# Performance work log

Hardware: AMD Instinct MI355X
Metric: run time of the kernel (lower is better)

Reference implementation:

```python
import jax, jax.numpy as jnp
import numpy as np

B, H, W, C, HEADS, SR = 4, 64, 64, 256, 8, 2
D = C // HEADS            # head dim = 32
SCALE = D ** -0.5
EPS = 1e-6


def _conv(x, w, stride, pad, groups):
    return jax.lax.conv_general_dilated(
        x, w, (stride, stride), [(pad, pad), (pad, pad)],
        feature_group_count=groups,
        dimension_numbers=('NCHW', 'OIHW', 'NCHW'))


def setup_inputs() -> dict:
    key = jax.random.key(0)
    ks = jax.random.split(key, 9)
    s = lambda fan: 1.0 / np.sqrt(fan)
    return {
        'x': jax.random.normal(ks[0], (B, H * W, C), jnp.float32),
        'dw_w': jax.random.normal(ks[1], (C, 1, 3, 3), jnp.float32) * s(9),
        'dw_b': jnp.zeros((C,), jnp.float32),
        'pw_w': jax.random.normal(ks[2], (C, C, 1, 1), jnp.float32) * s(C),
        'pw_b': jnp.zeros((C,), jnp.float32),
        'sr_w': jax.random.normal(ks[3], (C, 1, 3, 3), jnp.float32) * s(9),
        'ln_g': jnp.ones((C,), jnp.float32),
        'ln_b': jnp.zeros((C,), jnp.float32),
        'kv_w': jax.random.normal(ks[4], (2 * C, C), jnp.float32) * s(C),
        'kv_b': jnp.zeros((2 * C,), jnp.float32),
        'proj_w': jax.random.normal(ks[5], (C, C), jnp.float32) * s(C),
        'proj_b': jnp.zeros((C,), jnp.float32),
    }


def reference(x, dw_w, dw_b, pw_w, pw_b, sr_w, ln_g, ln_b, kv_w, kv_b, proj_w, proj_b):
    Bx, N, Cx = x.shape
    # Q path: depthwise-separable conv on the spatial layout
    xq = x.reshape(Bx, H, W, Cx).transpose(0, 3, 1, 2)          # (B,C,H,W)
    q = _conv(xq, dw_w, 1, 1, Cx) + dw_b[None, :, None, None]    # depthwise 3x3
    q = _conv(q, pw_w, 1, 0, 1) + pw_b[None, :, None, None]      # pointwise 1x1
    # 'b (h d) l w -> b h (l w) d'
    q = q.reshape(Bx, HEADS, D, H * W).transpose(0, 1, 3, 2)     # (B,h,N,d)

    # SR path for K/V: strided depthwise conv + LayerNorm
    x_ = _conv(xq, sr_w, SR, SR // 2, Cx)                        # (B,C,H/SR,W/SR)
    x_ = x_.reshape(Bx, Cx, -1).transpose(0, 2, 1)               # (B,M,C)
    mu = jnp.mean(x_, axis=-1, keepdims=True)
    var = jnp.mean(jnp.square(x_ - mu), axis=-1, keepdims=True)
    x_ = (x_ - mu) * jax.lax.rsqrt(var + EPS) * ln_g + ln_b

    kv = x_ @ kv_w.T + kv_b                                      # (B,M,2C)
    M = kv.shape[1]
    kv = kv.reshape(Bx, M, 2, HEADS, D).transpose(2, 0, 3, 1, 4) # (2,B,h,M,d)
    k, v = kv[0], kv[1]

    attn = jnp.einsum('bhnd,bhmd->bhnm', q, k) * SCALE           # (B,h,N,M)
    attn = jax.nn.softmax(attn, axis=-1)
    out = jnp.einsum('bhnm,bhmd->bhnd', attn, v)                 # (B,h,N,d)
    out = out.transpose(0, 2, 1, 3).reshape(Bx, N, Cx)           # (B,N,C)
    return out @ proj_w.T + proj_b
```

## Files before the change

### kernel.cpp

```cpp
#include <hip/hip_runtime.h>
#include <math.h>

#define BB 4
#define HH 64
#define WW 64
#define CC 256
#define NN 4096
#define MM 1024
#define LN_EPS 1e-6f
#define SLF (0.17677669529663687f * 1.4426950408889634f)

typedef __attribute__((ext_vector_type(8)))  short short8;
typedef __attribute__((ext_vector_type(8)))  _Float16 half8;
typedef __attribute__((ext_vector_type(16))) float f32x16;
typedef __attribute__((ext_vector_type(4)))  unsigned int uint32x4;

__device__ __forceinline__ ushort f2bf(float f) {
  unsigned u = __builtin_bit_cast(unsigned, f);
  u += 0x7fffu + ((u >> 16) & 1u);
  return (ushort)(u >> 16);
}
__device__ __forceinline__ float bf2f(ushort h) {
  unsigned u = ((unsigned)h) << 16;
  return __builtin_bit_cast(float, u);
}
__device__ __forceinline__ ushort f2h(float f) {
  return __builtin_bit_cast(ushort, (_Float16)f);
}
#if __has_builtin(__builtin_amdgcn_exp2f)
#define EXP2F(x) __builtin_amdgcn_exp2f(x)
#else
#define EXP2F(x) exp2f(x)
#endif

__global__ __launch_bounds__(256) void pre_fused(
    const float* __restrict__ x, const float* __restrict__ dw_w,
    const float* __restrict__ dw_b, const float* __restrict__ sr_w,
    const float* __restrict__ ln_g, const float* __restrict__ ln_b,
    const float* __restrict__ pw_w, const float* __restrict__ kv_w,
    const float* __restrict__ proj_w,
    ushort* __restrict__ q1b, ushort* __restrict__ xsr,
    ushort* __restrict__ pwB, ushort* __restrict__ kvB,
    ushort* __restrict__ pjH) {
  int bid = blockIdx.x;
  int c = threadIdx.x;
  if (bid < 4096) {
    int b = bid >> 10, m = bid & 1023;
    int my = m >> 5, mx = m & 31;
    const float* xb = x + (size_t)b * NN * CC + c;
    float acc = 0.f;
#pragma unroll
    for (int dy = 0; dy < 3; ++dy) {
      int iy = 2 * my + dy - 1;
      if (iy < 0 || iy >= HH) continue;
#pragma unroll
      for (int dx = 0; dx < 3; ++dx) {
        int ix = 2 * mx + dx - 1;
        if (ix < 0 || ix >= WW) continue;
        acc += xb[(size_t)(iy * WW + ix) * CC] * sr_w[c * 9 + dy * 3 + dx];
      }
    }
    float v1 = acc, v2 = acc * acc;
#pragma unroll
    for (int s = 1; s < 64; s <<= 1) {
      v1 += __shfl_xor(v1, s);
      v2 += __shfl_xor(v2, s);
    }
    __shared__ float r1[4], r2[4];
    int lane = c & 63, wv = c >> 6;
    if (lane == 0) { r1[wv] = v1; r2[wv] = v2; }
    __syncthreads();
    float s1 = r1[0] + r1[1] + r1[2] + r1[3];
    float s2 = r2[0] + r2[1] + r2[2] + r2[3];
    float mu = s1 * (1.f / 256.f);
    float var = s2 * (1.f / 256.f) - mu * mu;
    float yv = (acc - mu) * rsqrtf(var + LN_EPS) * ln_g[c] + ln_b[c];
    xsr[((size_t)b * MM + m) * CC + c] = f2bf(yv);
  } else if (bid < 6144) {
    int id = bid - 4096;
    int b = id >> 9, r = id & 511;
    int y = r >> 3, seg = r & 7;
    int x0 = seg * 8;
    float wr[9];
#pragma unroll
    for (int i = 0; i < 9; ++i) wr[i] = dw_w[c * 9 + i];
    float bi = dw_b[c];
    const float* xb = x + (size_t)b * NN * CC + c;
    bool okT = (y > 0), okB = (y < 63);
    float a0, a1, a2, b0, b1, b2;
    if (x0 == 0) {
      a0 = a1 = a2 = 0.f;
    } else {
      a0 = okT ? xb[(size_t)((y - 1) * 64 + x0 - 1) * CC] : 0.f;
      a1 = xb[(size_t)(y * 64 + x0 - 1) * CC];
      a2 = okB ? xb[(size_t)((y + 1) * 64 + x0 - 1) * CC] : 0.f;
    }
    b0 = okT ? xb[(size_t)((y - 1) * 64 + x0) * CC] : 0.f;
    b1 = xb[(size_t)(y * 64 + x0) * CC];
    b2 = okB ? xb[(size_t)((y + 1) * 64 + x0) * CC] : 0.f;
    ushort* ob = q1b + ((size_t)b * NN + y * 64) * CC + c;
#pragma unroll 8
    for (int xx = x0; xx < x0 + 8; ++xx) {
      float c0v, c1v, c2v;
      if (xx < 63) {
        c0v = okT ? xb[(size_t)((y - 1) * 64 + xx + 1) * CC] : 0.f;
        c1v = xb[(size_t)(y * 64 + xx + 1) * CC];
        c2v = okB ? xb[(size_t)((y + 1) * 64 + xx + 1) * CC] : 0.f;
      } else {
        c0v = c1v = c2v = 0.f;
      }
      float acc = bi;
      acc += a0 * wr[0] + b0 * wr[1] + c0v * wr[2];
      acc += a1 * wr[3] + b1 * wr[4] + c1v * wr[5];
      acc += a2 * wr[6] + b2 * wr[7] + c2v * wr[8];
      ob[(size_t)xx * CC] = f2bf(acc);
      a0 = b0; a1 = b1; a2 = b2;
      b0 = c0v; b1 = c1v; b2 = c2v;
    }
  } else if (bid < 6208) {
    int i0 = (bid - 6144) * 1024 + c * 4;
    float4 v = *(const float4*)&pw_w[i0];
    ushort tmp[4] = {f2bf(v.x), f2bf(v.y), f2bf(v.z), f2bf(v.w)};
    *(uint2*)&pwB[i0] = *(uint2*)tmp;
  } else if (bid < 6336) {
    int i0 = (bid - 6208) * 1024 + c * 4;
    float4 v = *(const float4*)&kv_w[i0];
    ushort tmp[4] = {f2bf(v.x), f2bf(v.y), f2bf(v.z), f2bf(v.w)};
    *(uint2*)&kvB[i0] = *(uint2*)tmp;
  } else {
    int i0 = (bid - 6336) * 1024 + c * 4;
    float4 v = *(const float4*)&proj_w[i0];
    ushort th[4] = {f2h(v.x), f2h(v.y), f2h(v.z), f2h(v.w)};
    *(uint2*)&pjH[i0] = *(uint2*)th;
  }
}

__global__ __launch_bounds__(256) void gemm_qkv(
    const ushort* __restrict__ q1b, const ushort* __restrict__ xsr,
    const ushort* __restrict__ pwB, const float* __restrict__ pw_b,
    const ushort* __restrict__ kvB, const float* __restrict__ kv_b,
    ushort* __restrict__ qB, ushort* __restrict__ kB,
    ushort* __restrict__ vT) {
  __shared__ ushort smem[2][128 * 40];
  int bid = blockIdx.x;
  bool is0 = bid < 1024;
  const ushort* A;
  const ushort* W;
  const float* bias;
  int r0, c0;
  if (is0) {
    A = q1b; W = pwB; bias = pw_b;
    r0 = (bid >> 2) * 64; c0 = (bid & 3) * 64;
  } else {
    int sid = bid - 1024;
    A = xsr; W = kvB; bias = kv_b;
    r0 = (sid >> 3) * 64; c0 = (sid & 7) * 64;
  }
  const bool vmode = (!is0) && (c0 >= 256);

  int t = threadIdx.x;
  int lane = t & 63, w = t >> 6;
  int l31 = lane & 31, half = lane >> 5;
  int wr = w >> 1, wc = w & 1;
  int rowA = t >> 2, kq = (t & 3) * 8;

  f32x16 acc;
#pragma unroll
  for (int i = 0; i < 16; ++i) acc[i] = 0.f;

  short8 ra[2], rw[2];
  auto prefetch = [&](int kc, int s) {
    ra[s] = *(const short8*)&A[(size_t)(r0 + rowA) * 256 + kc + kq];
    rw[s] = *(const short8*)&W[(size_t)(c0 + rowA) * 256 + kc + kq];
  };
  auto store = [&](ushort* buf, int s) {
    *(short8*)&buf[rowA * 40 + kq] = ra[s];
    *(short8*)&buf[64 * 40 + rowA * 40 + kq] = rw[s];
  };

  prefetch(0, 0);
  store(smem[0], 0);
  prefetch(32, 1);
  __syncthreads();
#pragma unroll
  for (int i = 0; i < 8; ++i) {
    ushort* cur = smem[i & 1];
    ushort* nxt = smem[(i & 1) ^ 1];
    if (i < 7) store(nxt, (i + 1) & 1);
    if (i < 6) prefetch((i + 2) * 32, i & 1);
#pragma unroll
    for (int ks = 0; ks < 2; ++ks) {
      short8 af = *(const short8*)&cur[(wr * 32 + l31) * 40 + ks * 16 + half * 8];
      short8 wf = *(const short8*)&cur[64 * 40 + (wc * 32 + l31) * 40 + ks * 16 + half * 8];
      if (vmode)
        acc = __builtin_amdgcn_mfma_f32_32x32x16_bf16(wf, af, acc, 0, 0, 0);
      else
        acc = __builtin_amdgcn_mfma_f32_32x32x16_bf16(af, wf, acc, 0, 0, 0);
    }
    __syncthreads();
  }

#pragma unroll
  for (int i = 0; i < 16; ++i) {
    int rl = (i & 3) + 8 * (i >> 2) + 4 * half;
    if (is0) {
      int r = r0 + wr * 32 + rl;
      int c = c0 + wc * 32 + l31;
      int b = r >> 12, n = r & 4095;
      int h = c >> 5, d = c & 31;
      qB[((size_t)(b * 8 + h) * NN + n) * 32 + d] =
          f2bf((acc[i] + bias[c]) * SLF);
    } else if (!vmode) {
      int r = r0 + wr * 32 + rl;
      int c = c0 + wc * 32 + l31;
      int b = r >> 10, m = r & 1023;
      int h = c >> 5, d = c & 31;
      kB[((size_t)(b * 8 + h) * MM + m) * 32 + d] = f2bf(acc[i] + bias[c]);
    } else {
      int c = c0 + wc * 32 + rl;
      int r = r0 + wr * 32 + l31;
      int b = r >> 10, m = r & 1023;
      int cv = c - 256;
      int h = cv >> 5, d = cv & 31;
      vT[((size_t)(b * 8 + h) * 32 + d) * MM + m] = f2bf(acc[i] + bias[c]);
    }
  }
}

__global__ __launch_bounds__(256, 4) void attn_mfma(
    const ushort* __restrict__ qB, const ushort* __restrict__ kB,
    const ushort* __restrict__ vT, ushort* __restrict__ aH) {
  __shared__ ushort sKa[2][8][264];
  __shared__ ushort sVa[2][8][264];
  __shared__ ushort tb[4][32][36];
  int t = threadIdx.x;
  int lane = t & 63, w = t >> 6;
  int l31 = lane & 31, half = lane >> 5;
  int bh = blockIdx.y;
  int b = bh >> 3, h = bh & 7;
  int q0 = blockIdx.x * 128;

  const ushort* qrow = qB + ((size_t)bh * NN + q0 + w * 32 + l31) * 32;
  short8 bq0 = *(const short8*)(qrow + half * 8);
  short8 bq1 = *(const short8*)(qrow + 16 + half * 8);

  const ushort* kbase = kB + (size_t)bh * MM * 32;
  const ushort* vbase = vT + (size_t)bh * 32 * MM;
  int krow = t >> 2, kq = (t & 3) * 8;
  int vd = t >> 3, vmo = (t & 7) * 8;
  int kreg_idx = (krow >> 5) * 4 + (kq >> 4) * 2 + ((kq >> 3) & 1);
  int klane = (krow & 31) * 8;
  int vreg_idx = (vmo >> 4) * 2 + ((vmo >> 3) & 1);
  int vlane = vd * 8;

  short8 kr[2], vr[2];
  kr[0] = *(const short8*)&kbase[(size_t)krow * 32 + kq];
  vr[0] = *(const short8*)&vbase[(size_t)vd * MM + vmo];
  kr[1] = *(const short8*)&kbase[(size_t)(64 + krow) * 32 + kq];
  vr[1] = *(const short8*)&vbase[(size_t)vd * MM + 64 + vmo];
  *(short8*)&sKa[0][kreg_idx][klane] = kr[0];
  *(short8*)&sVa[0][vreg_idx][vlane] = vr[0];

  f32x16 o;
#pragma unroll
  for (int i = 0; i < 16; ++i) o[i] = 0.f;
  float psum = 0.f;
  __syncthreads();

#pragma unroll 2
  for (int mc = 0; mc < 16; ++mc) {
    int cur = mc & 1, nxt = cur ^ 1;

    auto doTile = [&](int tt) {
      f32x16 z;
      __builtin_amdgcn_s_setprio(1);
      {
        short8 a0 = *(const short8*)&sKa[cur][tt * 4 + 0 + half][l31 * 8];
        short8 a1 = *(const short8*)&sKa[cur][tt * 4 + 2 + half][l31 * 8];
#pragma unroll
        for (int i = 0; i < 16; ++i) z[i] = 0.f;
        z = __builtin_amdgcn_mfma_f32_32x32x16_bf16(a0, bq0, z, 0, 0, 0);
        z = __builtin_amdgcn_mfma_f32_32x32x16_bf16(a1, bq1, z, 0, 0, 0);
      }
      __builtin_amdgcn_s_setprio(0);

      float e[16];
#pragma unroll
      for (int i = 0; i < 16; ++i) e[i] = EXP2F(z[i]);
#pragma unroll
      for (int i = 0; i < 16; i += 4)
        psum += (e[i] + e[i + 1]) + (e[i + 2] + e[i + 3]);
      unsigned pk[8];
#pragma unroll
      for (int j = 0; j < 8; ++j)
        asm("v_cvt_pk_bf16_f32 %0, %1, %2"
            : "=v"(pk[j]) : "v"(e[2 * j]), "v"(e[2 * j + 1]));
      __builtin_amdgcn_s_setprio(1);
#pragma unroll
      for (int kbl = 0; kbl < 2; ++kbl) {
        unsigned w0 = pk[4 * kbl + 0], w2 = pk[4 * kbl + 2];
        unsigned w1 = pk[4 * kbl + 1], w3 = pk[4 * kbl + 3];
        asm("v_permlane32_swap_b32 %0, %1" : "+v"(w0), "+v"(w2));
        asm("v_permlane32_swap_b32 %0, %1" : "+v"(w1), "+v"(w3));
        uint32x4 wbits = {w0, w1, w2, w3};
        short8 bp = __builtin_bit_cast(short8, wbits);
        int kb = 2 * tt + kbl;
        short8 av = *(const short8*)&sVa[cur][kb * 2 + half][l31 * 8];
        o = __builtin_amdgcn_mfma_f32_32x32x16_bf16(av, bp, o, 0, 0, 0);
      }
      __builtin_amdgcn_s_setprio(0);
    };

    doTile(0);

    if (mc < 15) {
      *(short8*)&sKa[nxt][kreg_idx][klane] = kr[nxt];
      *(short8*)&sVa[nxt][vreg_idx][vlane] = vr[nxt];
    }
    if (mc < 14) {
      int m2 = (mc + 2) * 64;
      kr[cur] = *(const short8*)&kbase[(size_t)(m2 + krow) * 32 + kq];
      vr[cur] = *(const short8*)&vbase[(size_t)vd * MM + m2 + vmo];
    }

    doTile(1);

    __syncthreads();
  }

  float denom = psum + __shfl_xor(psum, 32);
  float inv = 1.f / denom;
#pragma unroll
  for (int rg = 0; rg < 4; ++rg) {
    ushort h4[4];
#pragma unroll
    for (int j = 0; j < 4; ++j) h4[j] = f2h(o[rg * 4 + j] * inv);
    *(uint2*)&tb[w][l31][rg * 8 + half * 4] = *(uint2*)h4;
  }
  int rr = lane >> 3, cc = (lane & 7) * 4;
  size_t gb = ((size_t)b * NN + q0 + w * 32) * 256 + h * 32 + cc;
#pragma unroll
  for (int it = 0; it < 4; ++it) {
    int r = it * 8 + rr;
    uint2 v = *(uint2*)&tb[w][r][cc];
    *(uint2*)&aH[gb + (size_t)r * 256] = v;
  }
}

__global__ __launch_bounds__(256) void gemm_proj(
    const ushort* __restrict__ A, const ushort* __restrict__ Whi,
    const float* __restrict__ bias, float* __restrict__ out) {
  __shared__ ushort smem[2][2 * 64 * 40];
  constexpr int OA = 0, OW = 64 * 40;
  int bid = blockIdx.x;
  int r0 = (bid >> 2) * 64, c0 = (bid & 3) * 64;

  int t = threadIdx.x;
  int lane = t & 63, w = t >> 6;
  int l31 = lane & 31, half = lane >> 5;
  int wr = w >> 1, wc = w & 1;
  int rowA = t >> 2, kq = (t & 3) * 8;

  f32x16 acc;
#pragma unroll
  for (int i = 0; i < 16; ++i) acc[i] = 0.f;

  short8 ra[2], rwh[2];
  auto prefetch = [&](int kc, int s) {
    ra[s]  = *(const short8*)&A[(size_t)(r0 + rowA) * 256 + kc + kq];
    rwh[s] = *(const short8*)&Whi[(size_t)(c0 + rowA) * 256 + kc + kq];
  };
  auto store = [&](ushort* buf, int s) {
    *(short8*)&buf[OA + rowA * 40 + kq] = ra[s];
    *(short8*)&buf[OW + rowA * 40 + kq] = rwh[s];
  };

  prefetch(0, 0);
  store(smem[0], 0);
  prefetch(32, 1);
  __syncthreads();
#pragma unroll
  for (int i = 0; i < 8; ++i) {
    ushort* cur = smem[i & 1];
    ushort* nxt = smem[(i & 1) ^ 1];
    if (i < 7) store(nxt, (i + 1) & 1);
    if (i < 6) prefetch((i + 2) * 32, i & 1);
#pragma unroll
    for (int ks = 0; ks < 2; ++ks) {
      int ro = (wr * 32 + l31) * 40 + ks * 16 + half * 8;
      int co = (wc * 32 + l31) * 40 + ks * 16 + half * 8;
      half8 af = __builtin_bit_cast(half8, *(const short8*)&cur[OA + ro]);
      half8 wf = __builtin_bit_cast(half8, *(const short8*)&cur[OW + co]);
      acc = __builtin_amdgcn_mfma_f32_32x32x16_f16(af, wf, acc, 0, 0, 0);
    }
    __syncthreads();
  }

#pragma unroll
  for (int i = 0; i < 16; ++i) {
    int rl = (i & 3) + 8 * (i >> 2) + 4 * half;
    int r = r0 + wr * 32 + rl;
    int c = c0 + wc * 32 + l31;
    out[(size_t)r * 256 + c] = acc[i] + bias[c];
  }
}

extern "C" void kernel_launch(void* const* d_in, const int* in_sizes, int n_in,
                              void* d_out, int out_size, void* d_ws, size_t ws_size,
                              hipStream_t stream) {
  const float* x      = (const float*)d_in[0];
  const float* dw_w   = (const float*)d_in[1];
  const float* dw_b   = (const float*)d_in[2];
  const float* pw_w   = (const float*)d_in[3];
  const float* pw_b   = (const float*)d_in[4];
  const float* sr_w   = (const float*)d_in[5];
  const float* ln_g   = (const float*)d_in[6];
  const float* ln_b   = (const float*)d_in[7];
  const float* kv_w   = (const float*)d_in[8];
  const float* kv_b   = (const float*)d_in[9];
  const float* proj_w = (const float*)d_in[10];
  const float* proj_b = (const float*)d_in[11];
  float* out = (float*)d_out;

  char* ws = (char*)d_ws;
  ushort* q1b = (ushort*)(ws);
  ushort* xsr = (ushort*)(ws + (8u << 20));
  ushort* qB  = (ushort*)(ws + (16u << 20));
  ushort* kBp = (ushort*)(ws + (24u << 20));
  ushort* vTp = (ushort*)(ws + (26u << 20));
  ushort* aH  = (ushort*)(ws + (28u << 20));
  ushort* pwB = (ushort*)(ws + (44u << 20));
  ushort* kvB = (ushort*)(ws + (44u << 20) + (512u << 10));
  ushort* pjH = (ushort*)(ws + (45u << 20));

  pre_fused<<<dim3(6400), 256, 0, stream>>>(x, dw_w, dw_b, sr_w, ln_g, ln_b,
                                            pw_w, kv_w, proj_w,
                                            q1b, xsr, pwB, kvB, pjH);
  gemm_qkv<<<dim3(1536), 256, 0, stream>>>(q1b, xsr, pwB, pw_b, kvB, kv_b,
                                           qB, kBp, vTp);
  attn_mfma<<<dim3(32, 32), 256, 0, stream>>>(qB, kBp, vTp, aH);
  gemm_proj<<<dim3(1024), 256, 0, stream>>>(aH, pjH, proj_b, out);
}
```

Measured before the change: 146.1 us.

## Make attention waves independent: load K fragments directly, per-wave V staging

The attention kernel now runs 128-thread blocks, each wave handling 32 queries. K fragments are loaded straight from global memory into registers in MFMA operand layout rather than staged through shared memory. V is staged in a private per-wave double buffer, so all block-wide barriers are removed. This removes barrier stalls and shared-memory traffic for K, at the cost of more redundant global/L2 reads of K and V, since each wave fetches its own copy.

```diff
diff --git a/kernel.cpp b/kernel.cpp
--- a/kernel.cpp
+++ b/kernel.cpp
@@ -227,61 +227,58 @@
   }
 }
 
-__global__ __launch_bounds__(256, 4) void attn_mfma(
+__global__ __launch_bounds__(128, 4) void attn_mfma(
     const ushort* __restrict__ qB, const ushort* __restrict__ kB,
     const ushort* __restrict__ vT, ushort* __restrict__ aH) {
-  __shared__ ushort sKa[2][8][264];
-  __shared__ ushort sVa[2][8][264];
-  __shared__ ushort tb[4][32][36];
+  __shared__ ushort sV[2][2][8][264];
   int t = threadIdx.x;
-  int lane = t & 63, w = t >> 6;
+  int w = t >> 6, lane = t & 63;
   int l31 = lane & 31, half = lane >> 5;
   int bh = blockIdx.y;
   int b = bh >> 3, h = bh & 7;
-  int q0 = blockIdx.x * 128;
-
-  const ushort* qrow = qB + ((size_t)bh * NN + q0 + w * 32 + l31) * 32;
+  int q0 = blockIdx.x * 64 + w * 32;
+
+  const ushort* qrow = qB + ((size_t)bh * NN + q0 + l31) * 32;
   short8 bq0 = *(const short8*)(qrow + half * 8);
   short8 bq1 = *(const short8*)(qrow + 16 + half * 8);
 
   const ushort* kbase = kB + (size_t)bh * MM * 32;
   const ushort* vbase = vT + (size_t)bh * 32 * MM;
-  int krow = t >> 2, kq = (t & 3) * 8;
-  int vd = t >> 3, vmo = (t & 7) * 8;
-  int kreg_idx = (krow >> 5) * 4 + (kq >> 4) * 2 + ((kq >> 3) & 1);
-  int klane = (krow & 31) * 8;
-  int vreg_idx = (vmo >> 4) * 2 + ((vmo >> 3) & 1);
-  int vlane = vd * 8;
-
-  short8 kr[2], vr[2];
-  kr[0] = *(const short8*)&kbase[(size_t)krow * 32 + kq];
-  vr[0] = *(const short8*)&vbase[(size_t)vd * MM + vmo];
-  kr[1] = *(const short8*)&kbase[(size_t)(64 + krow) * 32 + kq];
-  vr[1] = *(const short8*)&vbase[(size_t)vd * MM + 64 + vmo];
-  *(short8*)&sKa[0][kreg_idx][klane] = kr[0];
-  *(short8*)&sVa[0][vreg_idx][vlane] = vr[0];
+  const ushort* kfp = kbase + (size_t)l31 * 32 + half * 8;
+  int vrow = lane >> 3, vcol = (lane & 7) * 8;
+  int vslot = lane & 7;
+
+  short8 ak[4], vr[4];
+  ak[0] = *(const short8*)(kfp);
+  ak[1] = *(const short8*)(kfp + 16);
+  ak[2] = *(const short8*)(kfp + 1024);
+  ak[3] = *(const short8*)(kfp + 1024 + 16);
+#pragma unroll
+  for (int j = 0; j < 4; ++j)
+    vr[j] = *(const short8*)&vbase[(size_t)(j * 8 + vrow) * MM + vcol];
+#pragma unroll
+  for (int j = 0; j < 4; ++j)
+    *(short8*)&sV[w][0][vslot][(j * 8 + vrow) * 8] = vr[j];
+#pragma unroll
+  for (int j = 0; j < 4; ++j)
+    vr[j] = *(const short8*)&vbase[(size_t)(j * 8 + vrow) * MM + 64 + vcol];
 
   f32x16 o;
 #pragma unroll
   for (int i = 0; i < 16; ++i) o[i] = 0.f;
   float psum = 0.f;
-  __syncthreads();
 
 #pragma unroll 2
   for (int mc = 0; mc < 16; ++mc) {
     int cur = mc & 1, nxt = cur ^ 1;
 
-    auto doTile = [&](int tt) {
+    auto doTile = [&](int tt, short8 a0, short8 a1) {
       f32x16 z;
       __builtin_amdgcn_s_setprio(1);
-      {
-        short8 a0 = *(const short8*)&sKa[cur][tt * 4 + 0 + half][l31 * 8];
-        short8 a1 = *(const short8*)&sKa[cur][tt * 4 + 2 + half][l31 * 8];
-#pragma unroll
-        for (int i = 0; i < 16; ++i) z[i] = 0.f;
-        z = __builtin_amdgcn_mfma_f32_32x32x16_bf16(a0, bq0, z, 0, 0, 0);
-        z = __builtin_amdgcn_mfma_f32_32x32x16_bf16(a1, bq1, z, 0, 0, 0);
-      }
+#pragma unroll
+      for (int i = 0; i < 16; ++i) z[i] = 0.f;
+      z = __builtin_amdgcn_mfma_f32_32x32x16_bf16(a0, bq0, z, 0, 0, 0);
+      z = __builtin_amdgcn_mfma_f32_32x32x16_bf16(a1, bq1, z, 0, 0, 0);
       __builtin_amdgcn_s_setprio(0);
 
       float e[16];
@@ -305,44 +302,53 @@
         uint32x4 wbits = {w0, w1, w2, w3};
         short8 bp = __builtin_bit_cast(short8, wbits);
         int kb = 2 * tt + kbl;
-        short8 av = *(const short8*)&sVa[cur][kb * 2 + half][l31 * 8];
+        short8 av = *(const short8*)&sV[w][cur][kb * 2 + half][l31 * 8];
         o = __builtin_amdgcn_mfma_f32_32x32x16_bf16(av, bp, o, 0, 0, 0);
       }
       __builtin_amdgcn_s_setprio(0);
     };
 
-    doTile(0);
-
     if (mc < 15) {
-      *(short8*)&sKa[nxt][kreg_idx][klane] = kr[nxt];
-      *(short8*)&sVa[nxt][vreg_idx][vlane] = vr[nxt];
+#pragma unroll
+      for (int j = 0; j < 4; ++j)
+        *(short8*)&sV[w][nxt][vslot][(j * 8 + vrow) * 8] = vr[j];
+    }
+    doTile(0, ak[0], ak[1]);
+    if (mc < 15) {
+      const ushort* kp = kfp + (size_t)(mc + 1) * 2048;
+      ak[0] = *(const short8*)(kp);
+      ak[1] = *(const short8*)(kp + 16);
     }
     if (mc < 14) {
-      int m2 = (mc + 2) * 64;
-      kr[cur] = *(const short8*)&kbase[(size_t)(m2 + krow) * 32 + kq];
-      vr[cur] = *(const short8*)&vbase[(size_t)vd * MM + m2 + vmo];
-    }
-
-    doTile(1);
-
-    __syncthreads();
+      size_t mo = (size_t)(mc + 2) * 64;
+#pragma unroll
+      for (int j = 0; j < 4; ++j)
+        vr[j] = *(const short8*)&vbase[(size_t)(j * 8 + vrow) * MM + mo + vcol];
+    }
+    doTile(1, ak[2], ak[3]);
+    if (mc < 15) {
+      const ushort* kp = kfp + (size_t)(mc + 1) * 2048 + 1024;
+      ak[2] = *(const short8*)(kp);
+      ak[3] = *(const short8*)(kp + 16);
+    }
   }
 
   float denom = psum + __shfl_xor(psum, 32);
   float inv = 1.f / denom;
+  ushort* tbw = (ushort*)&sV[w][0][0][0];
 #pragma unroll
   for (int rg = 0; rg < 4; ++rg) {
     ushort h4[4];
 #pragma unroll
     for (int j = 0; j < 4; ++j) h4[j] = f2h(o[rg * 4 + j] * inv);
-    *(uint2*)&tb[w][l31][rg * 8 + half * 4] = *(uint2*)h4;
+    *(uint2*)&tbw[l31 * 36 + rg * 8 + half * 4] = *(uint2*)h4;
   }
   int rr = lane >> 3, cc = (lane & 7) * 4;
-  size_t gb = ((size_t)b * NN + q0 + w * 32) * 256 + h * 32 + cc;
+  size_t gb = ((size_t)b * NN + q0) * 256 + h * 32 + cc;
 #pragma unroll
   for (int it = 0; it < 4; ++it) {
     int r = it * 8 + rr;
-    uint2 v = *(uint2*)&tb[w][r][cc];
+    uint2 v = *(uint2*)&tbw[r * 36 + cc];
     *(uint2*)&aH[gb + (size_t)r * 256] = v;
   }
 }
@@ -438,6 +444,6 @@
                                             q1b, xsr, pwB, kvB, pjH);
   gemm_qkv<<<dim3(1536), 256, 0, stream>>>(q1b, xsr, pwB, pw_b, kvB, kv_b,
                                            qB, kBp, vTp);
-  attn_mfma<<<dim3(32, 32), 256, 0, stream>>>(qB, kBp, vTp, aH);
+  attn_mfma<<<dim3(64, 32), 128, 0, stream>>>(qB, kBp, vTp, aH);
   gemm_proj<<<dim3(1024), 256, 0, stream>>>(aH, pjH, proj_b, out);
 }
```

Result: slower. 182.9 us (+25.2%).
